# Performance work log

Measured on AMD Instinct MI355X. Metric: run time of the kernel, lower is better.

Reference implementation:

```python
import jax, jax.numpy as jnp
import numpy as np

B, T, N, P2, K_S = 8, 64, 128, 256, 64

def setup_inputs() -> dict:
    key = jax.random.key(0)
    k1, k2, k3, k4 = jax.random.split(key, 4)
    x = jax.random.normal(k1, (B, T, N, P2), dtype=jnp.float32)
    W_Q = jax.random.uniform(k2, (P2, K_S), dtype=jnp.float32)
    W_K = jax.random.uniform(k3, (P2, K_S), dtype=jnp.float32)
    W_V = jax.random.uniform(k4, (P2, P2), dtype=jnp.float32)
    return {"x": x, "W_Q": W_Q, "W_K": W_K, "W_V": W_V}

def reference(x, W_Q, W_K, W_V):
    # x: [B, T, N, P2]
    q = jnp.einsum('btnp,pk->btnk', x, W_Q)          # [B,T,N,K_S]
    k = jnp.einsum('btnp,pk->btnk', x, W_K)          # [B,T,N,K_S]
    v = jnp.einsum('btnp,pq->btnq', x, W_V)          # [B,T,N,P2]
    scale = jnp.sqrt(jnp.asarray(K_S, dtype=x.dtype))
    scores = jnp.einsum('btik,btjk->btij', q, k) / scale  # [B,T,N,N]
    # NOTE: original uses nn.Softmax(dim=1) -> softmax over the T axis.
    attn = jax.nn.softmax(scores, axis=1)
    return jnp.einsum('btij,btjq->btiq', attn, v)    # [B,T,N,P2]
```

## Files before the change

### kernel.cpp

```cpp
#include <hip/hip_runtime.h>
#include <hip/hip_bf16.h>

#define Bv 8
#define Tv 64
#define Nv 128
#define P2v 256
#define KSv 64

typedef __attribute__((ext_vector_type(8))) short bf8;
typedef __attribute__((ext_vector_type(4))) float f4;

#define MFMA16(a, b, c) __builtin_amdgcn_mfma_f32_16x16x32_bf16((a), (b), (c), 0, 0, 0)

__device__ __forceinline__ unsigned short f2bf(float f) {
  unsigned u = __float_as_uint(f);
  return (unsigned short)((u + 0x7fffu + ((u >> 16) & 1u)) >> 16);
}
__device__ __forceinline__ float bf2f(unsigned short h) {
  return __uint_as_float(((unsigned)h) << 16);
}

__device__ __forceinline__ int swz64(int r, int c) {
  return r * 64 + ((((c >> 3)) ^ (r & 7)) << 3) + (c & 7);
}
__device__ __forceinline__ int swz32(int r, int c) {
  return r * 32 + ((((c >> 3)) ^ (r & 3)) << 3) + (c & 7);
}
__device__ __forceinline__ int swz128(int r, int c) {
  return r * 128 + ((((c >> 3)) ^ (r & 7)) << 3) + (c & 7);
}

__global__ __launch_bounds__(256) void prep_w_kernel(
    const float* __restrict__ Wq, const float* __restrict__ Wk,
    const float* __restrict__ Wv, unsigned short* __restrict__ wqh,
    unsigned short* __restrict__ wql, unsigned short* __restrict__ wkh,
    unsigned short* __restrict__ wkl, unsigned short* __restrict__ wvf) {
  const int e = blockIdx.x * 256 + threadIdx.x;
  if (e < 32768) {
    const float* W = (e < 16384) ? Wq : Wk;
    unsigned short* oh = (e < 16384) ? wqh : wkh;
    unsigned short* ol = (e < 16384) ? wql : wkl;
    const int t = e & 16383;
    const int jj = t & 7, lane = (t >> 3) & 63, nt = (t >> 9) & 3, pt = t >> 11;
    const int p = pt * 32 + 8 * (lane >> 4) + jj;
    const int n = nt * 16 + (lane & 15);
    const float v = W[p * KSv + n];
    const unsigned short h = f2bf(v);
    oh[t] = h;
    ol[t] = f2bf(v - bf2f(h));
  } else {
    const int t = e - 32768;
    const int jj = t & 7, lane = (t >> 3) & 63, nt = (t >> 9) & 15, pt = t >> 13;
    const int p = pt * 32 + 8 * (lane >> 4) + jj;
    const int q = nt * 16 + (lane & 15);
    wvf[t] = f2bf(Wv[p * P2v + q]);
  }
}

__global__ __launch_bounds__(512) void qk_kernel(
    const float* __restrict__ x, const unsigned short* __restrict__ wqh,
    const unsigned short* __restrict__ wql,
    const unsigned short* __restrict__ wkh,
    const unsigned short* __restrict__ wkl, float* __restrict__ S) {
  __shared__ alignas(16) unsigned short sh[4 * Nv * KSv];
  unsigned short* const xh_l = sh;
  unsigned short* const xl_l = sh + Nv * 32;
  unsigned short* const qh_l = sh;
  unsigned short* const ql_l = sh + 8192;
  unsigned short* const kh_l = sh + 16384;
  unsigned short* const kl_l = sh + 24576;
  const int bt = blockIdx.x;
  const float* __restrict__ X = x + (size_t)bt * (Nv * P2v);
  const int tid = threadIdx.x, lane = tid & 63, wid = tid >> 6;
  const int lg = lane >> 4, lr = lane & 15;
  const bool isQ = (wid < 4);
  const int nt = wid & 3;
  const unsigned short* __restrict__ wh = isQ ? wqh : wkh;
  const unsigned short* __restrict__ wl = isQ ? wql : wkl;

  const f4 zero = {0.f, 0.f, 0.f, 0.f};
  f4 acc[8];
#pragma unroll
  for (int rt = 0; rt < 8; ++rt) acc[rt] = zero;

  const int srow = tid >> 2;
  const int sp = (tid & 3) * 8;
  const float* __restrict__ Xrow = X + srow * P2v + sp;

  float4 pv0 = *(const float4*)(Xrow);
  float4 pv1 = *(const float4*)(Xrow + 4);
  bf8 pwh = *(const bf8*)(wh + (nt * 64 + lane) * 8);
  bf8 pwl = *(const bf8*)(wl + (nt * 64 + lane) * 8);

  for (int c = 0; c < 8; ++c) {
    ushort4 h0, l0, h1, l1;
    h0.x = f2bf(pv0.x); l0.x = f2bf(pv0.x - bf2f(h0.x));
    h0.y = f2bf(pv0.y); l0.y = f2bf(pv0.y - bf2f(h0.y));
    h0.z = f2bf(pv0.z); l0.z = f2bf(pv0.z - bf2f(h0.z));
    h0.w = f2bf(pv0.w); l0.w = f2bf(pv0.w - bf2f(h0.w));
    h1.x = f2bf(pv1.x); l1.x = f2bf(pv1.x - bf2f(h1.x));
    h1.y = f2bf(pv1.y); l1.y = f2bf(pv1.y - bf2f(h1.y));
    h1.z = f2bf(pv1.z); l1.z = f2bf(pv1.z - bf2f(h1.z));
    h1.w = f2bf(pv1.w); l1.w = f2bf(pv1.w - bf2f(h1.w));
    const bf8 cwh = pwh, cwl = pwl;

    __syncthreads();
    const int off = swz32(srow, sp);
    *(ushort4*)(xh_l + off) = h0;
    *(ushort4*)(xh_l + off + 4) = h1;
    *(ushort4*)(xl_l + off) = l0;
    *(ushort4*)(xl_l + off + 4) = l1;

    if (c < 7) {
      pv0 = *(const float4*)(Xrow + (c + 1) * 32);
      pv1 = *(const float4*)(Xrow + (c + 1) * 32 + 4);
      const int wo = (((c + 1) * 4 + nt) * 64 + lane) * 8;
      pwh = *(const bf8*)(wh + wo);
      pwl = *(const bf8*)(wl + wo);
    }
    __syncthreads();
#pragma unroll
    for (int rt = 0; rt < 8; ++rt) {
      const int xoff = swz32(rt * 16 + lr, lg * 8);
      const bf8 xh = *(const bf8*)(xh_l + xoff);
      const bf8 xl = *(const bf8*)(xl_l + xoff);
      acc[rt] = MFMA16(xh, cwh, acc[rt]);
      acc[rt] = MFMA16(xh, cwl, acc[rt]);
      acc[rt] = MFMA16(xl, cwh, acc[rt]);
    }
  }

  __syncthreads();

  unsigned short* const oh = isQ ? qh_l : kh_l;
  unsigned short* const ol = isQ ? ql_l : kl_l;
#pragma unroll
  for (int rt = 0; rt < 8; ++rt) {
#pragma unroll
    for (int rr = 0; rr < 4; ++rr) {
      const int i = rt * 16 + 4 * lg + rr;
      const int ks = nt * 16 + lr;
      const int off = swz64(i, ks);
      const float v = acc[rt][rr];
      const unsigned short h = f2bf(v);
      oh[off] = h;
      ol[off] = f2bf(v - bf2f(h));
    }
  }
  __syncthreads();

  const int r0 = wid * 16;
  f4 aS[8];
#pragma unroll
  for (int n = 0; n < 8; ++n) aS[n] = zero;
#pragma unroll
  for (int kt2 = 0; kt2 < 2; ++kt2) {
    const int qoff = swz64(r0 + lr, kt2 * 32 + lg * 8);
    const bf8 fqh = *(const bf8*)(qh_l + qoff);
    const bf8 fql = *(const bf8*)(ql_l + qoff);
#pragma unroll
    for (int n = 0; n < 8; ++n) {
      const int koff = swz64(n * 16 + lr, kt2 * 32 + lg * 8);
      const bf8 fkh = *(const bf8*)(kh_l + koff);
      const bf8 fkl = *(const bf8*)(kl_l + koff);
      aS[n] = MFMA16(fkh, fqh, aS[n]);
      aS[n] = MFMA16(fkl, fqh, aS[n]);
      aS[n] = MFMA16(fkh, fql, aS[n]);
    }
  }
  float* __restrict__ Sb = S + (size_t)bt * (Nv * Nv);
#pragma unroll
  for (int n = 0; n < 8; ++n) {
    float4 v;
    v.x = aS[n][0] * 0.125f;
    v.y = aS[n][1] * 0.125f;
    v.z = aS[n][2] * 0.125f;
    v.w = aS[n][3] * 0.125f;
    *(float4*)(Sb + (r0 + lr) * Nv + n * 16 + 4 * lg) = v;
  }
}

__global__ __launch_bounds__(256) void softmax_t_kernel(
    const float* __restrict__ S, unsigned short* __restrict__ Abf) {
  const int idx = blockIdx.x * 256 + threadIdx.x;
  const int j = idx & (Nv - 1);
  const int i = (idx >> 7) & (Nv - 1);
  const int b = idx >> 14;
  const size_t base = ((size_t)b * Tv * Nv * Nv) + (size_t)i * Nv + j;

  float vals[Tv];
  float m = -1e30f;
#pragma unroll
  for (int t = 0; t < Tv; ++t) {
    const float v = S[base + (size_t)t * Nv * Nv];
    vals[t] = v;
    m = fmaxf(m, v);
  }
  float s = 0.f;
#pragma unroll
  for (int t = 0; t < Tv; ++t) {
    const float e = __expf(vals[t] - m);
    vals[t] = e;
    s += e;
  }
  const float inv = 1.f / s;
#pragma unroll
  for (int t = 0; t < Tv; ++t) {
    Abf[base + (size_t)t * Nv * Nv] = f2bf(vals[t] * inv);
  }
}

__global__ __launch_bounds__(512) void av_kernel(
    const float* __restrict__ x, const unsigned short* __restrict__ wvf,
    const unsigned short* __restrict__ Abf, float* __restrict__ out) {
  __shared__ alignas(16) unsigned short xa[Nv * KSv];
  __shared__ alignas(16) unsigned short vth[Nv * Nv];
  const int bt = blockIdx.x;
  const float* __restrict__ X = x + (size_t)bt * (Nv * P2v);
  const unsigned short* __restrict__ Ab = Abf + (size_t)bt * (Nv * Nv);
  float* __restrict__ ob = out + (size_t)bt * (Nv * P2v);
  const int tid = threadIdx.x, lane = tid & 63, wid = tid >> 6;
  const int lg = lane >> 4, lr = lane & 15;
  const int r0 = wid * 16;

  const f4 zero = {0.f, 0.f, 0.f, 0.f};
  f4 aV[16];
#pragma unroll
  for (int n = 0; n < 16; ++n) aV[n] = zero;

  const int srow = tid >> 4;
  const int sp = (tid & 15) * 4;
  const float* __restrict__ Xrow = X + srow * P2v + sp;

  float4 pf0 = *(const float4*)(Xrow);
  float4 pf1 = *(const float4*)(Xrow + 32 * P2v);
  float4 pf2 = *(const float4*)(Xrow + 64 * P2v);
  float4 pf3 = *(const float4*)(Xrow + 96 * P2v);

  for (int c = 0; c < 4; ++c) {
    ushort4 q0, q1, q2, q3;
    q0.x = f2bf(pf0.x); q0.y = f2bf(pf0.y); q0.z = f2bf(pf0.z); q0.w = f2bf(pf0.w);
    q1.x = f2bf(pf1.x); q1.y = f2bf(pf1.y); q1.z = f2bf(pf1.z); q1.w = f2bf(pf1.w);
    q2.x = f2bf(pf2.x); q2.y = f2bf(pf2.y); q2.z = f2bf(pf2.z); q2.w = f2bf(pf2.w);
    q3.x = f2bf(pf3.x); q3.y = f2bf(pf3.y); q3.z = f2bf(pf3.z); q3.w = f2bf(pf3.w);

    __syncthreads();
    *(ushort4*)(xa + swz64(srow, sp)) = q0;
    *(ushort4*)(xa + swz64(srow + 32, sp)) = q1;
    *(ushort4*)(xa + swz64(srow + 64, sp)) = q2;
    *(ushort4*)(xa + swz64(srow + 96, sp)) = q3;

    if (c < 3) {
      pf0 = *(const float4*)(Xrow + (c + 1) * 64);
      pf1 = *(const float4*)(Xrow + (c + 1) * 64 + 32 * P2v);
      pf2 = *(const float4*)(Xrow + (c + 1) * 64 + 64 * P2v);
      pf3 = *(const float4*)(Xrow + (c + 1) * 64 + 96 * P2v);
    }
    __syncthreads();
#pragma unroll
    for (int ktl = 0; ktl < 2; ++ktl) {
      const int kt = c * 2 + ktl;
#pragma unroll
      for (int h = 0; h < 2; ++h) {
        const int ntile = h * 8 + wid;
        const int o = ((kt * 16 + ntile) * 64 + lane) * 8;
        const bf8 fv = *(const bf8*)(wvf + o);
#pragma unroll
        for (int rt = 0; rt < 8; ++rt) {
          const bf8 xh =
              *(const bf8*)(xa + swz64(rt * 16 + lr, ktl * 32 + lg * 8));
          aV[h * 8 + rt] = MFMA16(xh, fv, aV[h * 8 + rt]);
        }
      }
    }
  }

  bf8 af[4];
#pragma unroll
  for (int kt = 0; kt < 4; ++kt) {
    af[kt] = *(const bf8*)(Ab + (r0 + lr) * Nv + kt * 32 + lg * 8);
  }

#pragma unroll
  for (int h = 0; h < 2; ++h) {
    if (h == 1) __syncthreads();
    const int ql = wid * 16 + lr;
#pragma unroll
    for (int rt = 0; rt < 8; ++rt) {
      const int j0 = rt * 16 + 4 * lg;
      ushort4 pk;
      pk.x = f2bf(aV[h * 8 + rt][0]);
      pk.y = f2bf(aV[h * 8 + rt][1]);
      pk.z = f2bf(aV[h * 8 + rt][2]);
      pk.w = f2bf(aV[h * 8 + rt][3]);
      *(ushort4*)(vth + swz128(ql, j0)) = pk;
    }
    __syncthreads();

    f4 aO[8];
#pragma unroll
    for (int n = 0; n < 8; ++n) aO[n] = zero;
#pragma unroll
    for (int kt = 0; kt < 4; ++kt) {
#pragma unroll
      for (int n = 0; n < 8; ++n) {
        const bf8 vf =
            *(const bf8*)(vth + swz128(n * 16 + lr, kt * 32 + lg * 8));
        aO[n] = MFMA16(vf, af[kt], aO[n]);
      }
    }
#pragma unroll
    for (int n = 0; n < 8; ++n) {
      float4 v;
      v.x = aO[n][0];
      v.y = aO[n][1];
      v.z = aO[n][2];
      v.w = aO[n][3];
      *(float4*)(ob + (r0 + lr) * P2v + h * 128 + n * 16 + 4 * lg) = v;
    }
  }
}

extern "C" void kernel_launch(void* const* d_in, const int* in_sizes, int n_in,
                              void* d_out, int out_size, void* d_ws,
                              size_t ws_size, hipStream_t stream) {
  const float* x = (const float*)d_in[0];
  const float* Wq = (const float*)d_in[1];
  const float* Wk = (const float*)d_in[2];
  const float* Wv = (const float*)d_in[3];
  float* out = (float*)d_out;

  unsigned short* wqh = (unsigned short*)d_ws;
  unsigned short* wql = wqh + 16384;
  unsigned short* wkh = wql + 16384;
  unsigned short* wkl = wkh + 16384;
  unsigned short* wvf = wkl + 16384;
  float* S = (float*)((char*)d_ws + 262144);
  unsigned short* Abf = (unsigned short*)((char*)d_ws + 262144 + 33554432);

  hipLaunchKernelGGL(prep_w_kernel, dim3(384), dim3(256), 0, stream, Wq, Wk,
                     Wv, wqh, wql, wkh, wkl, wvf);
  hipLaunchKernelGGL(qk_kernel, dim3(Bv * Tv), dim3(512), 0, stream, x, wqh,
                     wql, wkh, wkl, S);
  hipLaunchKernelGGL(softmax_t_kernel, dim3(Bv * Nv * Nv / 256), dim3(256), 0,
                     stream, S, Abf);
  hipLaunchKernelGGL(av_kernel, dim3(Bv * Tv), dim3(512), 0, stream, x, wvf,
                     Abf, out);
}
```

Before: 80.63 us.

## Fuse softmax normalization into AV kernel and double-buffer x staging in LDS

The softmax kernel no longer writes the full normalized bf16 attention tensor. It now stores only the per-(b,i,j) max and reciprocal sum over T. The AV kernel reads raw scores plus these stats and computes exp/normalize in-register before the MFMA, which removes a 16MB bf16 write and its later read. Both the QK and AV kernels also switch to double-buffered LDS staging of x, so one barrier per chunk replaces two. The trade-off is recomputing exp in the AV kernel and reading fp32 scores (32MB) instead of bf16 attention (16MB), plus extra LDS use.

```diff
diff --git a/kernel.cpp b/kernel.cpp
--- a/kernel.cpp
+++ b/kernel.cpp
@@ -12,6 +12,11 @@
 
 #define MFMA16(a, b, c) __builtin_amdgcn_mfma_f32_16x16x32_bf16((a), (b), (c), 0, 0, 0)
 
+union B8U {
+  bf8 v;
+  short s[8];
+};
+
 __device__ __forceinline__ unsigned short f2bf(float f) {
   unsigned u = __float_as_uint(f);
   return (unsigned short)((u + 0x7fffu + ((u >> 16) & 1u)) >> 16);
@@ -28,6 +33,27 @@
 }
 __device__ __forceinline__ int swz128(int r, int c) {
   return r * 128 + ((((c >> 3)) ^ (r & 7)) << 3) + (c & 7);
+}
+
+__device__ __forceinline__ void cvt_hl(const float4& a, const float4& b,
+                                       ushort4& h0, ushort4& h1, ushort4& l0,
+                                       ushort4& l1) {
+  h0.x = f2bf(a.x); l0.x = f2bf(a.x - bf2f(h0.x));
+  h0.y = f2bf(a.y); l0.y = f2bf(a.y - bf2f(h0.y));
+  h0.z = f2bf(a.z); l0.z = f2bf(a.z - bf2f(h0.z));
+  h0.w = f2bf(a.w); l0.w = f2bf(a.w - bf2f(h0.w));
+  h1.x = f2bf(b.x); l1.x = f2bf(b.x - bf2f(h1.x));
+  h1.y = f2bf(b.y); l1.y = f2bf(b.y - bf2f(h1.y));
+  h1.z = f2bf(b.z); l1.z = f2bf(b.z - bf2f(h1.z));
+  h1.w = f2bf(b.w); l1.w = f2bf(b.w - bf2f(h1.w));
+}
+__device__ __forceinline__ ushort4 cvt_h(const float4& a) {
+  ushort4 h;
+  h.x = f2bf(a.x);
+  h.y = f2bf(a.y);
+  h.z = f2bf(a.z);
+  h.w = f2bf(a.w);
+  return h;
 }
 
 __global__ __launch_bounds__(256) void prep_w_kernel(
@@ -63,8 +89,6 @@
     const unsigned short* __restrict__ wkh,
     const unsigned short* __restrict__ wkl, float* __restrict__ S) {
   __shared__ alignas(16) unsigned short sh[4 * Nv * KSv];
-  unsigned short* const xh_l = sh;
-  unsigned short* const xl_l = sh + Nv * 32;
   unsigned short* const qh_l = sh;
   unsigned short* const ql_l = sh + 8192;
   unsigned short* const kh_l = sh + 16384;
@@ -86,50 +110,57 @@
   const int srow = tid >> 2;
   const int sp = (tid & 3) * 8;
   const float* __restrict__ Xrow = X + srow * P2v + sp;
+  const int soff = swz32(srow, sp);
 
   float4 pv0 = *(const float4*)(Xrow);
   float4 pv1 = *(const float4*)(Xrow + 4);
-  bf8 pwh = *(const bf8*)(wh + (nt * 64 + lane) * 8);
-  bf8 pwl = *(const bf8*)(wl + (nt * 64 + lane) * 8);
+  bf8 cwh = *(const bf8*)(wh + (nt * 64 + lane) * 8);
+  bf8 cwl = *(const bf8*)(wl + (nt * 64 + lane) * 8);
+  {
+    ushort4 h0, h1, l0, l1;
+    cvt_hl(pv0, pv1, h0, h1, l0, l1);
+    *(ushort4*)(sh + soff) = h0;
+    *(ushort4*)(sh + soff + 4) = h1;
+    *(ushort4*)(sh + 4096 + soff) = l0;
+    *(ushort4*)(sh + 4096 + soff + 4) = l1;
+  }
+  pv0 = *(const float4*)(Xrow + 32);
+  pv1 = *(const float4*)(Xrow + 36);
+  bf8 nwh = *(const bf8*)(wh + ((4 + nt) * 64 + lane) * 8);
+  bf8 nwl = *(const bf8*)(wl + ((4 + nt) * 64 + lane) * 8);
+  __syncthreads();
 
   for (int c = 0; c < 8; ++c) {
-    ushort4 h0, l0, h1, l1;
-    h0.x = f2bf(pv0.x); l0.x = f2bf(pv0.x - bf2f(h0.x));
-    h0.y = f2bf(pv0.y); l0.y = f2bf(pv0.y - bf2f(h0.y));
-    h0.z = f2bf(pv0.z); l0.z = f2bf(pv0.z - bf2f(h0.z));
-    h0.w = f2bf(pv0.w); l0.w = f2bf(pv0.w - bf2f(h0.w));
-    h1.x = f2bf(pv1.x); l1.x = f2bf(pv1.x - bf2f(h1.x));
-    h1.y = f2bf(pv1.y); l1.y = f2bf(pv1.y - bf2f(h1.y));
-    h1.z = f2bf(pv1.z); l1.z = f2bf(pv1.z - bf2f(h1.z));
-    h1.w = f2bf(pv1.w); l1.w = f2bf(pv1.w - bf2f(h1.w));
-    const bf8 cwh = pwh, cwl = pwl;
-
-    __syncthreads();
-    const int off = swz32(srow, sp);
-    *(ushort4*)(xh_l + off) = h0;
-    *(ushort4*)(xh_l + off + 4) = h1;
-    *(ushort4*)(xl_l + off) = l0;
-    *(ushort4*)(xl_l + off + 4) = l1;
-
-    if (c < 7) {
-      pv0 = *(const float4*)(Xrow + (c + 1) * 32);
-      pv1 = *(const float4*)(Xrow + (c + 1) * 32 + 4);
-      const int wo = (((c + 1) * 4 + nt) * 64 + lane) * 8;
-      pwh = *(const bf8*)(wh + wo);
-      pwl = *(const bf8*)(wl + wo);
-    }
-    __syncthreads();
+    const int rbase = (c & 1) * 8192;
 #pragma unroll
     for (int rt = 0; rt < 8; ++rt) {
-      const int xoff = swz32(rt * 16 + lr, lg * 8);
-      const bf8 xh = *(const bf8*)(xh_l + xoff);
-      const bf8 xl = *(const bf8*)(xl_l + xoff);
+      const int xoff = rbase + swz32(rt * 16 + lr, lg * 8);
+      const bf8 xh = *(const bf8*)(sh + xoff);
+      const bf8 xl = *(const bf8*)(sh + 4096 + xoff);
       acc[rt] = MFMA16(xh, cwh, acc[rt]);
       acc[rt] = MFMA16(xh, cwl, acc[rt]);
       acc[rt] = MFMA16(xl, cwh, acc[rt]);
     }
-  }
-
+    if (c < 7) {
+      cwh = nwh;
+      cwl = nwl;
+      ushort4 h0, h1, l0, l1;
+      cvt_hl(pv0, pv1, h0, h1, l0, l1);
+      const int wbase = ((c + 1) & 1) * 8192;
+      *(ushort4*)(sh + wbase + soff) = h0;
+      *(ushort4*)(sh + wbase + soff + 4) = h1;
+      *(ushort4*)(sh + wbase + 4096 + soff) = l0;
+      *(ushort4*)(sh + wbase + 4096 + soff + 4) = l1;
+      if (c < 6) {
+        pv0 = *(const float4*)(Xrow + (c + 2) * 32);
+        pv1 = *(const float4*)(Xrow + (c + 2) * 32 + 4);
+        const int wo = (((c + 2) * 4 + nt) * 64 + lane) * 8;
+        nwh = *(const bf8*)(wh + wo);
+        nwl = *(const bf8*)(wl + wo);
+      }
+      __syncthreads();
+    }
+  }
   __syncthreads();
 
   unsigned short* const oh = isQ ? qh_l : kh_l;
@@ -180,8 +211,9 @@
   }
 }
 
-__global__ __launch_bounds__(256) void softmax_t_kernel(
-    const float* __restrict__ S, unsigned short* __restrict__ Abf) {
+__global__ __launch_bounds__(256) void stats_t_kernel(
+    const float* __restrict__ S, float* __restrict__ M,
+    float* __restrict__ R) {
   const int idx = blockIdx.x * 256 + threadIdx.x;
   const int j = idx & (Nv - 1);
   const int i = (idx >> 7) & (Nv - 1);
@@ -199,25 +231,24 @@
   float s = 0.f;
 #pragma unroll
   for (int t = 0; t < Tv; ++t) {
-    const float e = __expf(vals[t] - m);
-    vals[t] = e;
-    s += e;
-  }
-  const float inv = 1.f / s;
-#pragma unroll
-  for (int t = 0; t < Tv; ++t) {
-    Abf[base + (size_t)t * Nv * Nv] = f2bf(vals[t] * inv);
-  }
+    s += __expf(vals[t] - m);
+  }
+  M[idx] = m;
+  R[idx] = 1.f / s;
 }
 
 __global__ __launch_bounds__(512) void av_kernel(
     const float* __restrict__ x, const unsigned short* __restrict__ wvf,
-    const unsigned short* __restrict__ Abf, float* __restrict__ out) {
-  __shared__ alignas(16) unsigned short xa[Nv * KSv];
+    const float* __restrict__ S, const float* __restrict__ M,
+    const float* __restrict__ R, float* __restrict__ out) {
+  __shared__ alignas(16) unsigned short xa[2 * Nv * KSv];
   __shared__ alignas(16) unsigned short vth[Nv * Nv];
   const int bt = blockIdx.x;
+  const int b = bt >> 6;
   const float* __restrict__ X = x + (size_t)bt * (Nv * P2v);
-  const unsigned short* __restrict__ Ab = Abf + (size_t)bt * (Nv * Nv);
+  const float* __restrict__ Sb = S + (size_t)bt * (Nv * Nv);
+  const float* __restrict__ Mb = M + (size_t)b * (Nv * Nv);
+  const float* __restrict__ Rb = R + (size_t)b * (Nv * Nv);
   float* __restrict__ ob = out + (size_t)bt * (Nv * P2v);
   const int tid = threadIdx.x, lane = tid & 63, wid = tid >> 6;
   const int lg = lane >> 4, lr = lane & 15;
@@ -236,27 +267,20 @@
   float4 pf1 = *(const float4*)(Xrow + 32 * P2v);
   float4 pf2 = *(const float4*)(Xrow + 64 * P2v);
   float4 pf3 = *(const float4*)(Xrow + 96 * P2v);
+  {
+    *(ushort4*)(xa + swz64(srow, sp)) = cvt_h(pf0);
+    *(ushort4*)(xa + swz64(srow + 32, sp)) = cvt_h(pf1);
+    *(ushort4*)(xa + swz64(srow + 64, sp)) = cvt_h(pf2);
+    *(ushort4*)(xa + swz64(srow + 96, sp)) = cvt_h(pf3);
+  }
+  pf0 = *(const float4*)(Xrow + 64);
+  pf1 = *(const float4*)(Xrow + 64 + 32 * P2v);
+  pf2 = *(const float4*)(Xrow + 64 + 64 * P2v);
+  pf3 = *(const float4*)(Xrow + 64 + 96 * P2v);
+  __syncthreads();
 
   for (int c = 0; c < 4; ++c) {
-    ushort4 q0, q1, q2, q3;
-    q0.x = f2bf(pf0.x); q0.y = f2bf(pf0.y); q0.z = f2bf(pf0.z); q0.w = f2bf(pf0.w);
-    q1.x = f2bf(pf1.x); q1.y = f2bf(pf1.y); q1.z = f2bf(pf1.z); q1.w = f2bf(pf1.w);
-    q2.x = f2bf(pf2.x); q2.y = f2bf(pf2.y); q2.z = f2bf(pf2.z); q2.w = f2bf(pf2.w);
-    q3.x = f2bf(pf3.x); q3.y = f2bf(pf3.y); q3.z = f2bf(pf3.z); q3.w = f2bf(pf3.w);
-
-    __syncthreads();
-    *(ushort4*)(xa + swz64(srow, sp)) = q0;
-    *(ushort4*)(xa + swz64(srow + 32, sp)) = q1;
-    *(ushort4*)(xa + swz64(srow + 64, sp)) = q2;
-    *(ushort4*)(xa + swz64(srow + 96, sp)) = q3;
-
-    if (c < 3) {
-      pf0 = *(const float4*)(Xrow + (c + 1) * 64);
-      pf1 = *(const float4*)(Xrow + (c + 1) * 64 + 32 * P2v);
-      pf2 = *(const float4*)(Xrow + (c + 1) * 64 + 64 * P2v);
-      pf3 = *(const float4*)(Xrow + (c + 1) * 64 + 96 * P2v);
-    }
-    __syncthreads();
+    const int rbase = (c & 1) * 8192;
 #pragma unroll
     for (int ktl = 0; ktl < 2; ++ktl) {
       const int kt = c * 2 + ktl;
@@ -267,18 +291,48 @@
         const bf8 fv = *(const bf8*)(wvf + o);
 #pragma unroll
         for (int rt = 0; rt < 8; ++rt) {
-          const bf8 xh =
-              *(const bf8*)(xa + swz64(rt * 16 + lr, ktl * 32 + lg * 8));
+          const bf8 xh = *(const bf8*)(
+              xa + rbase + swz64(rt * 16 + lr, ktl * 32 + lg * 8));
           aV[h * 8 + rt] = MFMA16(xh, fv, aV[h * 8 + rt]);
         }
       }
     }
+    if (c < 3) {
+      const int wbase = ((c + 1) & 1) * 8192;
+      *(ushort4*)(xa + wbase + swz64(srow, sp)) = cvt_h(pf0);
+      *(ushort4*)(xa + wbase + swz64(srow + 32, sp)) = cvt_h(pf1);
+      *(ushort4*)(xa + wbase + swz64(srow + 64, sp)) = cvt_h(pf2);
+      *(ushort4*)(xa + wbase + swz64(srow + 96, sp)) = cvt_h(pf3);
+      if (c < 2) {
+        pf0 = *(const float4*)(Xrow + (c + 2) * 64);
+        pf1 = *(const float4*)(Xrow + (c + 2) * 64 + 32 * P2v);
+        pf2 = *(const float4*)(Xrow + (c + 2) * 64 + 64 * P2v);
+        pf3 = *(const float4*)(Xrow + (c + 2) * 64 + 96 * P2v);
+      }
+      __syncthreads();
+    }
   }
 
   bf8 af[4];
 #pragma unroll
   for (int kt = 0; kt < 4; ++kt) {
-    af[kt] = *(const bf8*)(Ab + (r0 + lr) * Nv + kt * 32 + lg * 8);
+    const int o = (r0 + lr) * Nv + kt * 32 + lg * 8;
+    const float4 s0 = *(const float4*)(Sb + o);
+    const float4 s1 = *(const float4*)(Sb + o + 4);
+    const float4 m0 = *(const float4*)(Mb + o);
+    const float4 m1 = *(const float4*)(Mb + o + 4);
+    const float4 rv0 = *(const float4*)(Rb + o);
+    const float4 rv1 = *(const float4*)(Rb + o + 4);
+    B8U u;
+    u.s[0] = (short)f2bf(__expf(s0.x - m0.x) * rv0.x);
+    u.s[1] = (short)f2bf(__expf(s0.y - m0.y) * rv0.y);
+    u.s[2] = (short)f2bf(__expf(s0.z - m0.z) * rv0.z);
+    u.s[3] = (short)f2bf(__expf(s0.w - m0.w) * rv0.w);
+    u.s[4] = (short)f2bf(__expf(s1.x - m1.x) * rv1.x);
+    u.s[5] = (short)f2bf(__expf(s1.y - m1.y) * rv1.y);
+    u.s[6] = (short)f2bf(__expf(s1.z - m1.z) * rv1.z);
+    u.s[7] = (short)f2bf(__expf(s1.w - m1.w) * rv1.w);
+    af[kt] = u.v;
   }
 
 #pragma unroll
@@ -336,14 +390,15 @@
   unsigned short* wkl = wkh + 16384;
   unsigned short* wvf = wkl + 16384;
   float* S = (float*)((char*)d_ws + 262144);
-  unsigned short* Abf = (unsigned short*)((char*)d_ws + 262144 + 33554432);
+  float* M = (float*)((char*)d_ws + 262144 + 33554432);
+  float* R = M + Bv * Nv * Nv;
 
   hipLaunchKernelGGL(prep_w_kernel, dim3(384), dim3(256), 0, stream, Wq, Wk,
                      Wv, wqh, wql, wkh, wkl, wvf);
   hipLaunchKernelGGL(qk_kernel, dim3(Bv * Tv), dim3(512), 0, stream, x, wqh,
                      wql, wkh, wkl, S);
-  hipLaunchKernelGGL(softmax_t_kernel, dim3(Bv * Nv * Nv / 256), dim3(256), 0,
-                     stream, S, Abf);
-  hipLaunchKernelGGL(av_kernel, dim3(Bv * Tv), dim3(512), 0, stream, x, wvf,
-                     Abf, out);
-}
+  hipLaunchKernelGGL(stats_t_kernel, dim3(Bv * Nv * Nv / 256), dim3(256), 0,
+                     stream, S, M, R);
+  hipLaunchKernelGGL(av_kernel, dim3(Bv * Tv), dim3(512), 0, stream, x, wvf, S,
+                     M, R, out);
+}
```

Result: slower. 87.18 us (+8.1%).
